# Kernel optimization log

Measured on AMD Instinct MI355X. Metric: run time of the kernel, lower is better.

## Reference

```python
import jax, jax.numpy as jnp
import numpy as np

N = 50000      # num nodes
E = 800000     # edges per hypergraph (avg degree 16)
G = 3          # hyper_edge_num
D_IN = 128
D_OUT = 128


def setup_inputs() -> dict:
    key = jax.random.key(0)
    ks = jax.random.split(key, 6)
    company_emb = jax.random.normal(ks[0], (N, D_IN), dtype=jnp.float32)
    # nn.Linear weight [out, in], glorot-ish scaling
    W = jax.random.normal(ks[1], (D_OUT, D_IN), dtype=jnp.float32) / np.sqrt(D_IN).astype(np.float32)
    alpha = jax.random.normal(ks[2], (G, 1), dtype=jnp.float32)
    edge_rows = jax.random.randint(ks[3], (G, E), 0, N, dtype=jnp.int32)
    edge_cols = jax.random.randint(ks[4], (G, E), 0, N, dtype=jnp.int32)
    edge_vals = jax.random.normal(ks[5], (G, E), dtype=jnp.float32)
    return {
        "company_emb": company_emb,
        "W": W,
        "alpha": alpha,
        "edge_rows": edge_rows,
        "edge_cols": edge_cols,
        "edge_vals": edge_vals,
    }


def reference(company_emb, W, alpha, edge_rows, edge_cols, edge_vals):
    # shared dense projection: h = X @ W^T, [N, D_OUT]
    h = company_emb @ W.T

    def spmm(rows, cols, vals):
        # sparse Laplacian (COO) @ h : gather source rows, scale, scatter-add to dest rows
        msg = vals[:, None] * h[cols]                     # [E, D_OUT]
        return jax.ops.segment_sum(msg, rows, num_segments=N)

    aggs = jax.vmap(spmm)(edge_rows, edge_cols, edge_vals)  # [G, N, D_OUT]
    gate = jax.nn.sigmoid(alpha[:, 0])                       # [G]
    # res = sum_g sigmoid(alpha_g) * (L_g @ h)
    return jnp.einsum('g,gnd->nd', gate, aggs)
```

## Files before the change

### kernel.cpp

```cpp
#include <hip/hip_runtime.h>
#include <math.h>

#define NNODES 50000
#define NEDGE  800000
#define NG     3
#define GE     (NG*NEDGE)
#define NBUK   1536
#define OS     (NBUK + 1)
#define CH     4688
#define NBLK   512
#define GBLK   391
#define FGRID  (GBLK + NBLK)
#define STGCAP 1920
#define SCAP   2176

typedef __attribute__((ext_vector_type(8))) short bf16x8;
typedef __attribute__((ext_vector_type(4))) float f32x4;

__device__ __forceinline__ unsigned short f2bf(float f) {
    unsigned u = __float_as_uint(f);
    return (unsigned short)((u + 0x7fffu + ((u >> 16) & 1u)) >> 16);
}

__device__ __forceinline__ int bucket_of(unsigned r) {
    return (int)((r * 96u) / 3125u);
}

__global__ __launch_bounds__(512) void k_front(const float* __restrict__ X,
                                               const float* __restrict__ W,
                                               const int* __restrict__ rows,
                                               const int* __restrict__ cols,
                                               const float* __restrict__ vals,
                                               const float* __restrict__ alpha,
                                               unsigned short* __restrict__ hb16,
                                               uint2* __restrict__ out1,
                                               unsigned short* __restrict__ off1) {
    __shared__ __align__(16) char smem[53024];
    const int t = threadIdx.x;

    if (blockIdx.x < GBLK) {
        uint4* Wl = (uint4*)smem;
        for (int i = t; i < 2048; i += 512) {
            const int nt   = i >> 8;
            const int kc   = (i >> 6) & 3;
            const int lane = i & 63;
            const int n  = nt * 16 + (lane & 15);
            const int k0 = kc * 32 + (lane >> 4) * 8;
            const float* src = W + (size_t)n * 128 + k0;
            float4 a = *(const float4*)(src);
            float4 b = *(const float4*)(src + 4);
            unsigned u0 = (unsigned)f2bf(a.x) | ((unsigned)f2bf(a.y) << 16);
            unsigned u1 = (unsigned)f2bf(a.z) | ((unsigned)f2bf(a.w) << 16);
            unsigned u2 = (unsigned)f2bf(b.x) | ((unsigned)f2bf(b.y) << 16);
            unsigned u3 = (unsigned)f2bf(b.z) | ((unsigned)f2bf(b.w) << 16);
            Wl[i] = make_uint4(u0, u1, u2, u3);
        }
        __syncthreads();

        const int w    = t >> 6;
        const int lane = t & 63;
        const int q    = lane >> 4;
        const int ml   = lane & 15;
        const int m0   = blockIdx.x * 128 + w * 16;

        int xr = m0 + ml; if (xr >= NNODES) xr = NNODES - 1;
        const float* xrow = X + (size_t)xr * 128;

        bf16x8 xf[4];
#pragma unroll
        for (int kc = 0; kc < 4; ++kc) {
            const int k0 = kc * 32 + q * 8;
            float4 a = *(const float4*)(xrow + k0);
            float4 b = *(const float4*)(xrow + k0 + 4);
            bf16x8 v;
            v[0] = (short)f2bf(a.x); v[1] = (short)f2bf(a.y);
            v[2] = (short)f2bf(a.z); v[3] = (short)f2bf(a.w);
            v[4] = (short)f2bf(b.x); v[5] = (short)f2bf(b.y);
            v[6] = (short)f2bf(b.z); v[7] = (short)f2bf(b.w);
            xf[kc] = v;
        }

        f32x4 acc[8];
#pragma unroll
        for (int nt = 0; nt < 8; ++nt) acc[nt] = (f32x4){0.f, 0.f, 0.f, 0.f};
#pragma unroll
        for (int nt = 0; nt < 8; ++nt)
#pragma unroll
            for (int kc = 0; kc < 4; ++kc) {
                const bf16x8 wf = *(const bf16x8*)&Wl[(nt * 4 + kc) * 64 + lane];
                acc[nt] = __builtin_amdgcn_mfma_f32_16x16x32_bf16(xf[kc], wf, acc[nt], 0, 0, 0);
            }
        __syncthreads();

        unsigned short* hst = (unsigned short*)smem + w * 2176;
#pragma unroll
        for (int nt = 0; nt < 8; ++nt)
#pragma unroll
            for (int r = 0; r < 4; ++r)
                hst[(q * 4 + r) * 136 + nt * 16 + ml] = f2bf(acc[nt][r]);
        __syncthreads();

#pragma unroll
        for (int i = 0; i < 4; ++i) {
            const int chunk = i * 64 + lane;
            const int lr    = chunk >> 4;
            const int cc    = chunk & 15;
            const int row   = m0 + lr;
            const uint4 v = *(const uint4*)(hst + lr * 136 + cc * 8);
            if (row < NNODES)
                ((uint4*)(hb16 + (size_t)row * 128))[cc] = v;
        }
    } else {
        uint2*          stg = (uint2*)smem;
        unsigned short* rnk = (unsigned short*)(smem + 37504);
        int*            sA  = (int*)(smem + 46880);
        const int bb    = blockIdx.x - GBLK;
        const int start = bb * CH;
        const int end   = (start + CH < GE) ? (start + CH) : GE;
        const int len   = end - start;

        const float g0 = 1.0f / (1.0f + __expf(-alpha[0]));
        const float g1 = 1.0f / (1.0f + __expf(-alpha[1]));
        const float g2 = 1.0f / (1.0f + __expf(-alpha[2]));

#pragma unroll
        for (int j = 0; j < 3; ++j) sA[t + j * 512] = 0;
        __syncthreads();

        for (int k = t; k < len; k += 512) {
            const int idx = start + k;
            const int r = rows[idx];
            const int c = cols[idx];
            const float v = vals[idx];
            const float gv = v * (idx < NEDGE ? g0 : (idx < 2 * NEDGE ? g1 : g2));
            uint2 rec;
            rec.x = ((unsigned)r << 16) | (unsigned)c;
            rec.y = __float_as_uint(gv);
            stg[k] = rec;
            rnk[k] = (unsigned short)atomicAdd(&sA[bucket_of((unsigned)r)], 1);
        }
        __syncthreads();

        for (int off = 1; off < 1536; off <<= 1) {
            int v[3];
#pragma unroll
            for (int j = 0; j < 3; ++j) {
                const int i = t + j * 512;
                v[j] = sA[i] + ((i >= off) ? sA[i - off] : 0);
            }
            __syncthreads();
#pragma unroll
            for (int j = 0; j < 3; ++j) sA[t + j * 512] = v[j];
            __syncthreads();
        }

        if (t < NBUK) off1[(size_t)bb * OS + t] = (unsigned short)(t ? sA[t - 1] : 0);
        for (int b = t + 512; b < NBUK; b += 512)
            off1[(size_t)bb * OS + b] = (unsigned short)sA[b - 1];
        if (t == 0) off1[(size_t)bb * OS + NBUK] = (unsigned short)sA[NBUK - 1];

        for (int k = t; k < len; k += 512) {
            const uint2 rec = stg[k];
            const int b = bucket_of(rec.x >> 16);
            const int pos = (b ? sA[b - 1] : 0) + (int)rnk[k];
            out1[(size_t)bb * CH + pos] = rec;
        }
    }
}

__global__ __launch_bounds__(512, 8) void k_agg(const unsigned* __restrict__ hbits,
                                                const uint2* __restrict__ out1,
                                                const unsigned short* __restrict__ off1,
                                                float* __restrict__ out) {
    __shared__ __align__(16) uint2          stg[STGCAP];
    __shared__ __align__(16) unsigned short colS[SCAP];
    __shared__ __align__(16) float          valS[SCAP];
    __shared__ int rh[40], rbase[40], rcur[40];
    __shared__ int sA[512];
    const int t = threadIdx.x;
    const int b = blockIdx.x;

    const int sstart = (b * 3125 + 95) / 96;
    const int send   = ((b + 1) * 3125 + 95) / 96;
    const int width  = send - sstart;

    if (t < 40) rh[t] = 0;

    const int s0 = off1[(size_t)t * OS + b];
    const int e0 = off1[(size_t)t * OS + b + 1];
    const int len = e0 - s0;
    sA[t] = len;
    __syncthreads();

    for (int off = 1; off < 512; off <<= 1) {
        const int v = sA[t] + ((t >= off) ? sA[t - off] : 0);
        __syncthreads();
        sA[t] = v;
        __syncthreads();
    }
    const int base = sA[t] - len;

    {
        const uint2* seg = out1 + (size_t)t * CH;
        int p = base;
        for (int i = s0; i < e0; ++i, ++p) {
            const uint2 rec = seg[i];
            if (p < STGCAP) {
                stg[p] = rec;
                atomicAdd(&rh[(int)(rec.x >> 16) - sstart], 1);
            }
        }
    }
    __syncthreads();

    if (t < 64) sA[t] = (t < width) ? ((rh[t] + 7) & ~7) : 0;
    __syncthreads();
    for (int off = 1; off < 64; off <<= 1) {
        int v = 0;
        if (t < 64) v = sA[t] + ((t >= off) ? sA[t - off] : 0);
        __syncthreads();
        if (t < 64) sA[t] = v;
        __syncthreads();
    }
    if (t < width) {
        const int c  = rh[t];
        const int c8 = (c + 7) & ~7;
        const int rb = sA[t] - c8;
        rbase[t] = rb;
        rcur[t]  = rb;
        for (int k = rb + c; k < rb + c8; ++k) { colS[k] = 0; valS[k] = 0.f; }
    }
    __syncthreads();

    {
        const int lim = (base + len < STGCAP) ? (base + len) : STGCAP;
        for (int k = base; k < lim; ++k) {
            const uint2 rec = stg[k];
            const int lr  = (int)(rec.x >> 16) - sstart;
            const int pos = atomicAdd(&rcur[lr], 1);
            colS[pos] = (unsigned short)(rec.x & 0xffffu);
            valS[pos] = __uint_as_float(rec.y);
        }
    }
    __syncthreads();

    const int w    = t >> 6;
    const int lane = t & 63;
    for (int lr = w; lr < width; lr += 8) {
        const int s    = rbase[lr];
        const int cnt8 = (rh[lr] + 7) & ~7;
        float2 acc = make_float2(0.f, 0.f);
        int i = 0;
        for (; i + 16 <= cnt8; i += 16) {
            const uint4  c0 = *(const uint4*)&colS[s + i];
            const uint4  c1 = *(const uint4*)&colS[s + i + 8];
            const float4 v0 = *(const float4*)&valS[s + i];
            const float4 v1 = *(const float4*)&valS[s + i + 4];
            const float4 v2 = *(const float4*)&valS[s + i + 8];
            const float4 v3 = *(const float4*)&valS[s + i + 12];
            unsigned hb[16];
            hb[0]  = hbits[(size_t)(c0.x & 0xffffu) * 64 + lane];
            hb[1]  = hbits[(size_t)(c0.x >> 16)     * 64 + lane];
            hb[2]  = hbits[(size_t)(c0.y & 0xffffu) * 64 + lane];
            hb[3]  = hbits[(size_t)(c0.y >> 16)     * 64 + lane];
            hb[4]  = hbits[(size_t)(c0.z & 0xffffu) * 64 + lane];
            hb[5]  = hbits[(size_t)(c0.z >> 16)     * 64 + lane];
            hb[6]  = hbits[(size_t)(c0.w & 0xffffu) * 64 + lane];
            hb[7]  = hbits[(size_t)(c0.w >> 16)     * 64 + lane];
            hb[8]  = hbits[(size_t)(c1.x & 0xffffu) * 64 + lane];
            hb[9]  = hbits[(size_t)(c1.x >> 16)     * 64 + lane];
            hb[10] = hbits[(size_t)(c1.y & 0xffffu) * 64 + lane];
            hb[11] = hbits[(size_t)(c1.y >> 16)     * 64 + lane];
            hb[12] = hbits[(size_t)(c1.z & 0xffffu) * 64 + lane];
            hb[13] = hbits[(size_t)(c1.z >> 16)     * 64 + lane];
            hb[14] = hbits[(size_t)(c1.w & 0xffffu) * 64 + lane];
            hb[15] = hbits[(size_t)(c1.w >> 16)     * 64 + lane];
            const float vv[16] = {v0.x, v0.y, v0.z, v0.w, v1.x, v1.y, v1.z, v1.w,
                                  v2.x, v2.y, v2.z, v2.w, v3.x, v3.y, v3.z, v3.w};
#pragma unroll
            for (int j = 0; j < 16; ++j) {
                acc.x += vv[j] * __uint_as_float(hb[j] << 16);
                acc.y += vv[j] * __uint_as_float(hb[j] & 0xffff0000u);
            }
        }
        if (i < cnt8) {
            const uint4  c0 = *(const uint4*)&colS[s + i];
            const float4 v0 = *(const float4*)&valS[s + i];
            const float4 v1 = *(const float4*)&valS[s + i + 4];
            unsigned hb[8];
            hb[0] = hbits[(size_t)(c0.x & 0xffffu) * 64 + lane];
            hb[1] = hbits[(size_t)(c0.x >> 16)     * 64 + lane];
            hb[2] = hbits[(size_t)(c0.y & 0xffffu) * 64 + lane];
            hb[3] = hbits[(size_t)(c0.y >> 16)     * 64 + lane];
            hb[4] = hbits[(size_t)(c0.z & 0xffffu) * 64 + lane];
            hb[5] = hbits[(size_t)(c0.z >> 16)     * 64 + lane];
            hb[6] = hbits[(size_t)(c0.w & 0xffffu) * 64 + lane];
            hb[7] = hbits[(size_t)(c0.w >> 16)     * 64 + lane];
            const float vv[8] = {v0.x, v0.y, v0.z, v0.w, v1.x, v1.y, v1.z, v1.w};
#pragma unroll
            for (int j = 0; j < 8; ++j) {
                acc.x += vv[j] * __uint_as_float(hb[j] << 16);
                acc.y += vv[j] * __uint_as_float(hb[j] & 0xffff0000u);
            }
        }
        const int row = sstart + lr;
        ((float2*)out)[(size_t)row * 64 + lane] = acc;
    }
}

extern "C" void kernel_launch(void* const* d_in, const int* in_sizes, int n_in,
                              void* d_out, int out_size, void* d_ws, size_t ws_size,
                              hipStream_t stream) {
    const float* X     = (const float*)d_in[0];
    const float* W     = (const float*)d_in[1];
    const float* alpha = (const float*)d_in[2];
    const int*   rows  = (const int*)d_in[3];
    const int*   cols  = (const int*)d_in[4];
    const float* vals  = (const float*)d_in[5];
    float* out = (float*)d_out;

    char* ws = (char*)d_ws;
    unsigned*       hbits = (unsigned*)(ws + 0);
    unsigned short* hb16  = (unsigned short*)(ws + 0);
    uint2*          out1  = (uint2*)(ws + 12800000);
    unsigned short* off1  = (unsigned short*)(ws + 32002048);

    hipLaunchKernelGGL(k_front, dim3(FGRID), dim3(512), 0, stream,
                       X, W, rows, cols, vals, alpha, hb16, out1, off1);
    hipLaunchKernelGGL(k_agg, dim3(NBUK), dim3(512), 0, stream,
                       hbits, out1, off1, out);
}
```

Before: 219.3 us.

## Group edges by source-column phase so all warps gather from the same column range

```diff
diff --git a/kernel.cpp b/kernel.cpp
--- a/kernel.cpp
+++ b/kernel.cpp
@@ -12,7 +12,9 @@
 #define GBLK   391
 #define FGRID  (GBLK + NBLK)
 #define STGCAP 1920
-#define SCAP   2176
+#define NPH    7
+#define MAXG   231
+#define SCAP   2624
 
 typedef __attribute__((ext_vector_type(8))) short bf16x8;
 typedef __attribute__((ext_vector_type(4))) float f32x4;
@@ -175,7 +177,7 @@
     __shared__ __align__(16) uint2          stg[STGCAP];
     __shared__ __align__(16) unsigned short colS[SCAP];
     __shared__ __align__(16) float          valS[SCAP];
-    __shared__ int rh[40], rbase[40], rcur[40];
+    __shared__ int rh[MAXG], grpBase[MAXG + 1], gcur[MAXG];
     __shared__ int sA[512];
     const int t = threadIdx.x;
     const int b = blockIdx.x;
@@ -183,8 +185,9 @@
     const int sstart = (b * 3125 + 95) / 96;
     const int send   = ((b + 1) * 3125 + 95) / 96;
     const int width  = send - sstart;
-
-    if (t < 40) rh[t] = 0;
+    const int ngrp   = NPH * width;
+
+    if (t < MAXG) rh[t] = 0;
 
     const int s0 = off1[(size_t)t * OS + b];
     const int e0 = off1[(size_t)t * OS + b + 1];
@@ -199,6 +202,7 @@
         __syncthreads();
     }
     const int base = sA[t] - len;
+    __syncthreads();
 
     {
         const uint2* seg = out1 + (size_t)t * CH;
@@ -207,37 +211,43 @@
             const uint2 rec = seg[i];
             if (p < STGCAP) {
                 stg[p] = rec;
-                atomicAdd(&rh[(int)(rec.x >> 16) - sstart], 1);
+                const int lr = (int)(rec.x >> 16) - sstart;
+                const int ph = (int)((rec.x & 0xffffu) >> 13);
+                atomicAdd(&rh[ph * width + lr], 1);
             }
         }
     }
     __syncthreads();
 
-    if (t < 64) sA[t] = (t < width) ? ((rh[t] + 7) & ~7) : 0;
-    __syncthreads();
-    for (int off = 1; off < 64; off <<= 1) {
+    if (t < 256) sA[t] = (t < ngrp) ? ((rh[t] + 3) & ~3) : 0;
+    __syncthreads();
+    for (int off = 1; off < 256; off <<= 1) {
         int v = 0;
-        if (t < 64) v = sA[t] + ((t >= off) ? sA[t - off] : 0);
-        __syncthreads();
-        if (t < 64) sA[t] = v;
-        __syncthreads();
-    }
-    if (t < width) {
-        const int c  = rh[t];
-        const int c8 = (c + 7) & ~7;
-        const int rb = sA[t] - c8;
-        rbase[t] = rb;
-        rcur[t]  = rb;
-        for (int k = rb + c; k < rb + c8; ++k) { colS[k] = 0; valS[k] = 0.f; }
-    }
+        if (t < 256) v = sA[t] + ((t >= off) ? sA[t - off] : 0);
+        __syncthreads();
+        if (t < 256) sA[t] = v;
+        __syncthreads();
+    }
+    if (t < ngrp) {
+        const int pc = (rh[t] + 3) & ~3;
+        const int gb = sA[t] - pc;
+        grpBase[t] = gb;
+        gcur[t]    = gb;
+        for (int k = gb + rh[t]; k < gb + pc; ++k) { colS[k] = 0; valS[k] = 0.f; }
+    }
+    if (t == 0) grpBase[MAXG] = 0;
+    if (t == 256 - 1) {  }
+    __syncthreads();
+    if (t == 0) grpBase[ngrp] = sA[ngrp - 1];
     __syncthreads();
 
     {
         const int lim = (base + len < STGCAP) ? (base + len) : STGCAP;
         for (int k = base; k < lim; ++k) {
             const uint2 rec = stg[k];
-            const int lr  = (int)(rec.x >> 16) - sstart;
-            const int pos = atomicAdd(&rcur[lr], 1);
+            const int lr = (int)(rec.x >> 16) - sstart;
+            const int ph = (int)((rec.x & 0xffffu) >> 13);
+            const int pos = atomicAdd(&gcur[ph * width + lr], 1);
             colS[pos] = (unsigned short)(rec.x & 0xffffu);
             valS[pos] = __uint_as_float(rec.y);
         }
@@ -246,65 +256,66 @@
 
     const int w    = t >> 6;
     const int lane = t & 63;
-    for (int lr = w; lr < width; lr += 8) {
-        const int s    = rbase[lr];
-        const int cnt8 = (rh[lr] + 7) & ~7;
-        float2 acc = make_float2(0.f, 0.f);
-        int i = 0;
-        for (; i + 16 <= cnt8; i += 16) {
-            const uint4  c0 = *(const uint4*)&colS[s + i];
-            const uint4  c1 = *(const uint4*)&colS[s + i + 8];
-            const float4 v0 = *(const float4*)&valS[s + i];
-            const float4 v1 = *(const float4*)&valS[s + i + 4];
-            const float4 v2 = *(const float4*)&valS[s + i + 8];
-            const float4 v3 = *(const float4*)&valS[s + i + 12];
-            unsigned hb[16];
-            hb[0]  = hbits[(size_t)(c0.x & 0xffffu) * 64 + lane];
-            hb[1]  = hbits[(size_t)(c0.x >> 16)     * 64 + lane];
-            hb[2]  = hbits[(size_t)(c0.y & 0xffffu) * 64 + lane];
-            hb[3]  = hbits[(size_t)(c0.y >> 16)     * 64 + lane];
-            hb[4]  = hbits[(size_t)(c0.z & 0xffffu) * 64 + lane];
-            hb[5]  = hbits[(size_t)(c0.z >> 16)     * 64 + lane];
-            hb[6]  = hbits[(size_t)(c0.w & 0xffffu) * 64 + lane];
-            hb[7]  = hbits[(size_t)(c0.w >> 16)     * 64 + lane];
-            hb[8]  = hbits[(size_t)(c1.x & 0xffffu) * 64 + lane];
-            hb[9]  = hbits[(size_t)(c1.x >> 16)     * 64 + lane];
-            hb[10] = hbits[(size_t)(c1.y & 0xffffu) * 64 + lane];
-            hb[11] = hbits[(size_t)(c1.y >> 16)     * 64 + lane];
-            hb[12] = hbits[(size_t)(c1.z & 0xffffu) * 64 + lane];
-            hb[13] = hbits[(size_t)(c1.z >> 16)     * 64 + lane];
-            hb[14] = hbits[(size_t)(c1.w & 0xffffu) * 64 + lane];
-            hb[15] = hbits[(size_t)(c1.w >> 16)     * 64 + lane];
-            const float vv[16] = {v0.x, v0.y, v0.z, v0.w, v1.x, v1.y, v1.z, v1.w,
-                                  v2.x, v2.y, v2.z, v2.w, v3.x, v3.y, v3.z, v3.w};
-#pragma unroll
-            for (int j = 0; j < 16; ++j) {
-                acc.x += vv[j] * __uint_as_float(hb[j] << 16);
-                acc.y += vv[j] * __uint_as_float(hb[j] & 0xffff0000u);
+    float2 acc[5];
+#pragma unroll
+    for (int ri = 0; ri < 5; ++ri) acc[ri] = make_float2(0.f, 0.f);
+
+    for (int ph = 0; ph < NPH; ++ph) {
+#pragma unroll
+        for (int ri = 0; ri < 5; ++ri) {
+            const int lr = w + ri * 8;
+            if (lr < width) {
+                const int g = ph * width + lr;
+                const int s = grpBase[g];
+                const int e = grpBase[g + 1];
+                int i = s;
+                for (; i + 8 <= e; i += 8) {
+                    const uint2  ca = *(const uint2*)&colS[i];
+                    const uint2  cb = *(const uint2*)&colS[i + 4];
+                    const float4 v0 = *(const float4*)&valS[i];
+                    const float4 v1 = *(const float4*)&valS[i + 4];
+                    unsigned hb[8];
+                    hb[0] = hbits[(size_t)(ca.x & 0xffffu) * 64 + lane];
+                    hb[1] = hbits[(size_t)(ca.x >> 16)     * 64 + lane];
+                    hb[2] = hbits[(size_t)(ca.y & 0xffffu) * 64 + lane];
+                    hb[3] = hbits[(size_t)(ca.y >> 16)     * 64 + lane];
+                    hb[4] = hbits[(size_t)(cb.x & 0xffffu) * 64 + lane];
+                    hb[5] = hbits[(size_t)(cb.x >> 16)     * 64 + lane];
+                    hb[6] = hbits[(size_t)(cb.y & 0xffffu) * 64 + lane];
+                    hb[7] = hbits[(size_t)(cb.y >> 16)     * 64 + lane];
+                    const float vv[8] = {v0.x, v0.y, v0.z, v0.w, v1.x, v1.y, v1.z, v1.w};
+#pragma unroll
+                    for (int j = 0; j < 8; ++j) {
+                        acc[ri].x += vv[j] * __uint_as_float(hb[j] << 16);
+                        acc[ri].y += vv[j] * __uint_as_float(hb[j] & 0xffff0000u);
+                    }
+                }
+                if (i < e) {
+                    const uint2  ca = *(const uint2*)&colS[i];
+                    const float4 v0 = *(const float4*)&valS[i];
+                    unsigned hb[4];
+                    hb[0] = hbits[(size_t)(ca.x & 0xffffu) * 64 + lane];
+                    hb[1] = hbits[(size_t)(ca.x >> 16)     * 64 + lane];
+                    hb[2] = hbits[(size_t)(ca.y & 0xffffu) * 64 + lane];
+                    hb[3] = hbits[(size_t)(ca.y >> 16)     * 64 + lane];
+                    const float vv[4] = {v0.x, v0.y, v0.z, v0.w};
+#pragma unroll
+                    for (int j = 0; j < 4; ++j) {
+                        acc[ri].x += vv[j] * __uint_as_float(hb[j] << 16);
+                        acc[ri].y += vv[j] * __uint_as_float(hb[j] & 0xffff0000u);
+                    }
+                }
             }
         }
-        if (i < cnt8) {
-            const uint4  c0 = *(const uint4*)&colS[s + i];
-            const float4 v0 = *(const float4*)&valS[s + i];
-            const float4 v1 = *(const float4*)&valS[s + i + 4];
-            unsigned hb[8];
-            hb[0] = hbits[(size_t)(c0.x & 0xffffu) * 64 + lane];
-            hb[1] = hbits[(size_t)(c0.x >> 16)     * 64 + lane];
-            hb[2] = hbits[(size_t)(c0.y & 0xffffu) * 64 + lane];
-            hb[3] = hbits[(size_t)(c0.y >> 16)     * 64 + lane];
-            hb[4] = hbits[(size_t)(c0.z & 0xffffu) * 64 + lane];
-            hb[5] = hbits[(size_t)(c0.z >> 16)     * 64 + lane];
-            hb[6] = hbits[(size_t)(c0.w & 0xffffu) * 64 + lane];
-            hb[7] = hbits[(size_t)(c0.w >> 16)     * 64 + lane];
-            const float vv[8] = {v0.x, v0.y, v0.z, v0.w, v1.x, v1.y, v1.z, v1.w};
-#pragma unroll
-            for (int j = 0; j < 8; ++j) {
-                acc.x += vv[j] * __uint_as_float(hb[j] << 16);
-                acc.y += vv[j] * __uint_as_float(hb[j] & 0xffff0000u);
-            }
-        }
-        const int row = sstart + lr;
-        ((float2*)out)[(size_t)row * 64 + lane] = acc;
+    }
+
+#pragma unroll
+    for (int ri = 0; ri < 5; ++ri) {
+        const int lr = w + ri * 8;
+        if (lr < width) {
+            const int row = sstart + lr;
+            ((float2*)out)[(size_t)row * 64 + lane] = acc[ri];
+        }
     }
 }
 
```

Result: faster. 212.8 us (-2.9%).
